# Performance work log

Measured on AMD Instinct MI355X. Metric: run time of the kernel, lower is better.

The kernel has to match this reference:

```python
import jax, jax.numpy as jnp
import numpy as np

B, T, C, H, E, K, F = 2, 2048, 1024, 16, 8, 2, 2048  # batch, seq, d_model, heads, experts, top_k, d_ffn
EPS = 1e-5


def setup_inputs() -> dict:
    key = jax.random.key(0)
    ks = jax.random.split(key, 6)
    s = 0.02
    return {
        "x": jax.random.normal(ks[0], (B, T, C), jnp.float32),
        "ln1_w": jnp.ones((C,), jnp.float32),
        "c_attn_w": jax.random.normal(ks[1], (C, 3 * C), jnp.float32) * s,
        "c_proj_w": jax.random.normal(ks[2], (C, C), jnp.float32) * s,
        "ln2_w": jnp.ones((C,), jnp.float32),
        "router_w": jax.random.normal(ks[3], (C, E), jnp.float32) * s,
        "w1": jnp.clip(jax.random.normal(ks[4], (C, E * F), jnp.float32) * s, -0.06, 0.06),
        "w2": jnp.clip(jax.random.normal(ks[5], (E * F, C), jnp.float32) * s, -0.06, 0.06),
    }


def layernorm(x, w):
    m = x.mean(-1, keepdims=True)
    v = x.var(-1, keepdims=True)
    return (x - m) * jax.lax.rsqrt(v + EPS) * w


def attention(x, c_attn_w, c_proj_w):
    b, t, c = x.shape
    hd = c // H
    q, k, v = jnp.split(x @ c_attn_w, 3, axis=-1)
    q = q.reshape(b, t, H, hd).transpose(0, 2, 1, 3)  # bhtd
    k = k.reshape(b, t, H, hd).transpose(0, 2, 1, 3)
    v = v.reshape(b, t, H, hd).transpose(0, 2, 1, 3)
    att = jnp.einsum('bhqd,bhkd->bhqk', q, k) / jnp.sqrt(jnp.asarray(hd, x.dtype))
    causal = jnp.tril(jnp.ones((t, t), bool))
    att = jnp.where(causal, att, jnp.asarray(-jnp.inf, att.dtype))
    att = jax.nn.softmax(att, axis=-1)
    y = jnp.einsum('bhqk,bhkd->bhqd', att, v)
    y = y.transpose(0, 2, 1, 3).reshape(b, t, c)
    return y @ c_proj_w


def moe_mlp(x, router_w, w1, w2):
    b, t, c = x.shape
    xf = x.reshape(-1, c)  # (N, C), N = b*t
    router_logits = xf @ router_w  # (N, E)
    probs = jax.nn.softmax(router_logits.astype(jnp.float32), axis=-1)
    rw, sel = jax.lax.top_k(probs, K)  # (N, K)
    rw = rw / rw.sum(axis=-1, keepdims=True)  # norm_topk_prob=True
    rw = rw.astype(x.dtype)
    # expert e uses w1[:, e*F:(e+1)*F] and w2[e*F:(e+1)*F, :]
    w1e = w1.reshape(c, E, F).transpose(1, 0, 2)  # (E, C, F)
    w2e = w2.reshape(E, F, c)  # (E, F, C)
    h = jax.nn.gelu(jnp.einsum('nc,ecf->enf', xf, w1e), approximate=False)
    y_all = jnp.einsum('enf,efc->nec', h, w2e)  # (N, E, C)
    y_sel = jnp.take_along_axis(y_all, sel[:, :, None], axis=1)  # (N, K, C)
    y = (y_sel * rw[:, :, None]).sum(axis=1)
    return y.reshape(b, t, c)


def reference(x, ln1_w, c_attn_w, c_proj_w, ln2_w, router_w, w1, w2):
    x = x + attention(layernorm(x, ln1_w), c_attn_w, c_proj_w)
    x = x + moe_mlp(layernorm(x, ln2_w), router_w, w1, w2)
    return x
```

## Files before the change

### kernel.cpp

```cpp
#include <hip/hip_runtime.h>
#include <hip/hip_bf16.h>

#define BB 2
#define TT 2048
#define CCH 1024
#define HH 16
#define HD 64
#define EE 8
#define FF 2048
#define NTOK (BB*TT)

typedef __bf16 bf16x8 __attribute__((ext_vector_type(8)));
typedef float f32x4 __attribute__((ext_vector_type(4)));
typedef unsigned int u32;
typedef const u32 __attribute__((address_space(1)))* gads;
typedef u32 __attribute__((address_space(3)))* lads;

static __device__ __forceinline__ unsigned short f2bf(float f) {
  union { float f; unsigned u; } v; v.f = f;
  unsigned u = v.u;
  u += 0x7fffu + ((u >> 16) & 1u);
  return (unsigned short)(u >> 16);
}
static __device__ __forceinline__ float bf2f(unsigned short h) {
  union { unsigned u; float f; } v; v.u = ((unsigned)h) << 16;
  return v.f;
}

__global__ __launch_bounds__(256) void k_transpose(const float* __restrict__ in,
    unsigned short* __restrict__ out, int R, int Cc) {
  __shared__ float tile[32][33];
  size_t zoff = (size_t)blockIdx.z * (size_t)R * (size_t)Cc;
  int r0 = blockIdx.y * 32, c0 = blockIdx.x * 32;
  int tx = threadIdx.x, ty = threadIdx.y;
#pragma unroll
  for (int ii = 0; ii < 4; ++ii) {
    int i = ty + ii * 8;
    tile[i][tx] = in[zoff + (size_t)(r0 + i) * Cc + c0 + tx];
  }
  __syncthreads();
#pragma unroll
  for (int ii = 0; ii < 4; ++ii) {
    int i = ty + ii * 8;
    out[zoff + (size_t)(c0 + i) * R + r0 + tx] = f2bf(tile[tx][i]);
  }
}

__global__ __launch_bounds__(256) void k_ln(const float* __restrict__ x,
    const float* __restrict__ w, unsigned short* __restrict__ out) {
  int row = blockIdx.x;
  const float* xr = x + (size_t)row * CCH;
  int tid = threadIdx.x;
  float4 v = *(const float4*)&xr[tid * 4];
  float s = v.x + v.y + v.z + v.w;
  float ss = v.x * v.x + v.y * v.y + v.z * v.z + v.w * v.w;
#pragma unroll
  for (int off = 32; off; off >>= 1) { s += __shfl_xor(s, off); ss += __shfl_xor(ss, off); }
  __shared__ float red[8];
  int wv = tid >> 6, l = tid & 63;
  if (l == 0) { red[wv] = s; red[4 + wv] = ss; }
  __syncthreads();
  s = red[0] + red[1] + red[2] + red[3];
  ss = red[4] + red[5] + red[6] + red[7];
  float mean = s * (1.f / CCH);
  float var = ss * (1.f / CCH) - mean * mean;
  float inv = rsqrtf(var + 1e-5f);
  float4 w4 = *(const float4*)&w[tid * 4];
  ushort4 o;
  o.x = f2bf((v.x - mean) * inv * w4.x);
  o.y = f2bf((v.y - mean) * inv * w4.y);
  o.z = f2bf((v.z - mean) * inv * w4.z);
  o.w = f2bf((v.w - mean) * inv * w4.w);
  *(ushort4*)&out[(size_t)row * CCH + tid * 4] = o;
}

#define CSP 140
#define CFP 70
template<int EPI>
__global__ __launch_bounds__(256, 4) void k_gemm128(
    const unsigned short* __restrict__ A, const unsigned short* __restrict__ BT,
    unsigned short* __restrict__ Cb, float* __restrict__ Cf,
    const float* __restrict__ resid, int M, int N, int K,
    const int* __restrict__ tokarr, const int* __restrict__ slotarr,
    const float* __restrict__ wgtarr, const int* __restrict__ offs,
    const int* __restrict__ counts, const int* __restrict__ tmap)
{
  __shared__ __align__(16) char pool[35840];
  unsigned short* As = (unsigned short*)pool;
  unsigned short* Bs = (unsigned short*)(pool + 16384);

  int mb, nb, e = 0, off = 0, cnt = M;
  if (EPI >= 2) {
    int tm = blockIdx.x;
    if (tm >= tmap[8]) return;
    e = 0;
    while (tm >= tmap[e + 1]) ++e;
    mb = tm - tmap[e];
    nb = blockIdx.y;
    cnt = counts[e]; off = offs[e];
  } else {
    int gx = gridDim.x, gy = gridDim.y;
    int nwg = gx * gy;
    int orig = blockIdx.y * gx + blockIdx.x;
    int q = nwg >> 3, r = nwg & 7;
    int xcd = orig & 7, idx = orig >> 3;
    int wk = (xcd < r ? xcd * (q + 1) : r * (q + 1) + (xcd - r) * q) + idx;
    nb = wk % gy; mb = wk / gy;
  }
  int m0 = mb * 128, n0 = nb * 128;

  int tid = threadIdx.x, l = tid & 63, w = tid >> 6;
  int scol = (((l & 7) ^ ((l >> 3) & 7)) * 8);
  const unsigned short* aptr[4];
  const unsigned short* bptr[4];
  const unsigned short* bbase = BT + (size_t)e * (size_t)N * K;
#pragma unroll
  for (int i = 0; i < 4; ++i) {
    int row = (w * 4 + i) * 8 + (l >> 3);
    int ra;
    if (EPI == 2)      ra = tokarr[off + min(m0 + row, cnt - 1)];
    else if (EPI == 3) ra = off + min(m0 + row, cnt - 1);
    else               ra = m0 + row;
    aptr[i] = A + (size_t)ra * K + scol;
    bptr[i] = bbase + (size_t)(n0 + row) * K + scol;
  }

  int wr = (w >> 1) * 64, wc = (w & 1) * 64;
  int frow = l & 15;
  int fkB = (l >> 4) * 16;
  int swz = (frow & 7) << 4;
  f32x4 acc[4][4] = {};

  for (int k0 = 0; k0 < K; k0 += 64) {
#pragma unroll
    for (int i = 0; i < 4; ++i) {
      int j = w * 4 + i;
      __builtin_amdgcn_global_load_lds((gads)(const void*)(aptr[i] + k0),
                                       (lads)(void*)(As + j * 512), 16, 0, 0);
      __builtin_amdgcn_global_load_lds((gads)(const void*)(bptr[i] + k0),
                                       (lads)(void*)(Bs + j * 512), 16, 0, 0);
    }
    __syncthreads();
    const char* ab = (const char*)As;
    const char* bb = (const char*)Bs;
#pragma unroll
    for (int kk = 0; kk < 2; ++kk) {
      int inr = (kk * 64 + fkB) ^ swz;
      bf16x8 af[4], bfr[4];
#pragma unroll
      for (int mi = 0; mi < 4; ++mi)
        af[mi] = *(const bf16x8*)(ab + (wr + mi * 16 + frow) * 128 + inr);
#pragma unroll
      for (int ni = 0; ni < 4; ++ni)
        bfr[ni] = *(const bf16x8*)(bb + (wc + ni * 16 + frow) * 128 + inr);
#pragma unroll
      for (int mi = 0; mi < 4; ++mi)
#pragma unroll
        for (int ni = 0; ni < 4; ++ni)
          acc[mi][ni] = __builtin_amdgcn_mfma_f32_16x16x32_bf16(af[mi], bfr[ni],
                                                                acc[mi][ni], 0, 0, 0);
    }
    __syncthreads();
  }

  int g4 = (l >> 4) * 4, cl = l & 15;

  if (EPI == 0 || EPI == 2) {
    unsigned short* Cs = (unsigned short*)pool;
#pragma unroll
    for (int mi = 0; mi < 4; ++mi)
#pragma unroll
      for (int ni = 0; ni < 4; ++ni)
#pragma unroll
        for (int r2 = 0; r2 < 4; ++r2) {
          float v = acc[mi][ni][r2];
          if (EPI == 2) v = 0.5f * v * (1.f + erff(v * 0.70710678118654752f));
          Cs[(wr + mi * 16 + g4 + r2) * CSP + wc + ni * 16 + cl] = f2bf(v);
        }
    __syncthreads();
    int row = tid >> 1, c0 = (tid & 1) * 64;
    if (EPI == 0 || m0 + row < cnt) {
      size_t grow = (EPI == 2) ? (size_t)(off + m0 + row) : (size_t)(m0 + row);
      unsigned short* dst = Cb + grow * N + n0 + c0;
#pragma unroll
      for (int j = 0; j < 8; ++j)
        ((uint4*)dst)[j] = *(const uint4*)&Cs[row * CSP + c0 + j * 8];
    }
  } else {
    float* Csf = (float*)pool;
#pragma unroll
    for (int p = 0; p < 2; ++p) {
      __syncthreads();
      if ((w & 1) == p) {
#pragma unroll
        for (int mi = 0; mi < 4; ++mi)
#pragma unroll
          for (int ni = 0; ni < 4; ++ni)
#pragma unroll
            for (int r2 = 0; r2 < 4; ++r2)
              Csf[(wr + mi * 16 + g4 + r2) * CFP + ni * 16 + cl] = acc[mi][ni][r2];
      }
      __syncthreads();
      int row = tid >> 1, c0 = (tid & 1) * 32;
      int gcol = n0 + p * 64 + c0;
      if (EPI == 1) {
        float* dst = Cf + (size_t)(m0 + row) * N + gcol;
        const float* rsd = resid + (size_t)(m0 + row) * N + gcol;
#pragma unroll
        for (int j = 0; j < 8; ++j) {
          float4 v = *(const float4*)&Csf[row * CFP + c0 + j * 4];
          float4 rr = ((const float4*)rsd)[j];
          v.x += rr.x; v.y += rr.y; v.z += rr.z; v.w += rr.w;
          ((float4*)dst)[j] = v;
        }
      } else {
        if (m0 + row < cnt) {
          int fl = off + m0 + row;
          int tok = tokarr[fl], slot = slotarr[fl];
          float wg = wgtarr[fl];
          float* dst = Cf + ((size_t)tok * 2 + slot) * N + gcol;
#pragma unroll
          for (int j = 0; j < 8; ++j) {
            float4 v = *(const float4*)&Csf[row * CFP + c0 + j * 4];
            v.x *= wg; v.y *= wg; v.z *= wg; v.w *= wg;
            ((float4*)dst)[j] = v;
          }
        }
      }
    }
  }
}

__global__ __launch_bounds__(256) void k_attn_mfma(const unsigned short* __restrict__ qkv,
    unsigned short* __restrict__ yout)
{
  int bx = blockIdx.x, h = blockIdx.y, b = blockIdx.z;
  int tid = threadIdx.x, l = tid & 63, w = tid >> 6;
  const size_t rs = 3 * CCH;
  const int NTILE = TT / 64;

  __shared__ __align__(16) unsigned short Ks[64][72];
  __shared__ __align__(16) unsigned short Vt[64][72];
  __shared__ __align__(16) unsigned short Ps[4][16][72];

  int frow = l & 15, fk = (l >> 4) * 8;
  int g4 = l >> 4;
  int kr = tid >> 2, kc0 = (tid & 3) * 8;
  int vr = tid >> 2, vc0 = (tid & 3) * 16;

  for (int half = 0; half < 2; ++half) {
    int qt = half ? (NTILE - 1 - bx) : bx;
    int q0 = qt * 64;

    const unsigned short* qp = qkv + (size_t)((size_t)b * TT + q0 + w * 16 + frow) * rs + h * HD;
    bf16x8 qf0 = *(const bf16x8*)&qp[fk];
    bf16x8 qf1 = *(const bf16x8*)&qp[32 + fk];

    f32x4 oacc[4] = {};
    float mrow[4] = {-INFINITY, -INFINITY, -INFINITY, -INFINITY};
    float lrow[4] = {};

    for (int kb = 0; kb <= qt; ++kb) {
      int k0 = kb * 64;
      __syncthreads();
      const unsigned short* kp = qkv + (size_t)((size_t)b * TT + k0 + kr) * rs + CCH + h * HD;
      *(uint4*)&Ks[kr][kc0]      = *(const uint4*)&kp[kc0];
      *(uint4*)&Ks[kr][kc0 + 32] = *(const uint4*)&kp[kc0 + 32];
      const unsigned short* vp = qkv + (size_t)((size_t)b * TT + k0 + vr) * rs + 2 * CCH + h * HD + vc0;
      uint4 v0 = *(const uint4*)&vp[0];
      uint4 v1 = *(const uint4*)&vp[8];
      unsigned short tmp[16];
      *(uint4*)&tmp[0] = v0; *(uint4*)&tmp[8] = v1;
#pragma unroll
      for (int j = 0; j < 16; ++j) Vt[vc0 + j][vr] = tmp[j];
      __syncthreads();

      f32x4 sacc[4] = {};
#pragma unroll
      for (int nb = 0; nb < 4; ++nb) {
        bf16x8 kf0 = *(const bf16x8*)&Ks[nb * 16 + frow][fk];
        bf16x8 kf1 = *(const bf16x8*)&Ks[nb * 16 + frow][32 + fk];
        sacc[nb] = __builtin_amdgcn_mfma_f32_16x16x32_bf16(qf0, kf0, sacc[nb], 0, 0, 0);
        sacc[nb] = __builtin_amdgcn_mfma_f32_16x16x32_bf16(qf1, kf1, sacc[nb], 0, 0, 0);
      }

      bool diag = (kb == qt);
      float sv[4][4];
#pragma unroll
      for (int nb = 0; nb < 4; ++nb)
#pragma unroll
        for (int r = 0; r < 4; ++r) {
          float v = sacc[nb][r] * 0.125f;
          if (diag) {
            int ckv = nb * 16 + frow;
            int rq = w * 16 + 4 * g4 + r;
            if (ckv > rq) v = -INFINITY;
          }
          sv[nb][r] = v;
        }
      float fscale[4];
#pragma unroll
      for (int r = 0; r < 4; ++r) {
        float vm = fmaxf(fmaxf(sv[0][r], sv[1][r]), fmaxf(sv[2][r], sv[3][r]));
        vm = fmaxf(vm, __shfl_xor(vm, 1));
        vm = fmaxf(vm, __shfl_xor(vm, 2));
        vm = fmaxf(vm, __shfl_xor(vm, 4));
        vm = fmaxf(vm, __shfl_xor(vm, 8));
        float mnew = fmaxf(mrow[r], vm);
        float f = __expf(mrow[r] - mnew);
        mrow[r] = mnew;
        fscale[r] = f;
        float psum = 0.f;
#pragma unroll
        for (int nb = 0; nb < 4; ++nb) {
          float p = __expf(sv[nb][r] - mnew);
          sv[nb][r] = p;
          psum += p;
        }
        psum += __shfl_xor(psum, 1);
        psum += __shfl_xor(psum, 2);
        psum += __shfl_xor(psum, 4);
        psum += __shfl_xor(psum, 8);
        lrow[r] = lrow[r] * f + psum;
      }
#pragma unroll
      for (int nb = 0; nb < 4; ++nb)
#pragma unroll
        for (int r = 0; r < 4; ++r) {
          oacc[nb][r] *= fscale[r];
          Ps[w][4 * g4 + r][nb * 16 + frow] = f2bf(sv[nb][r]);
        }
#pragma unroll
      for (int ks = 0; ks < 2; ++ks) {
        bf16x8 pa = *(const bf16x8*)&Ps[w][frow][ks * 32 + fk];
#pragma unroll
        for (int nb = 0; nb < 4; ++nb) {
          bf16x8 vb = *(const bf16x8*)&Vt[nb * 16 + frow][ks * 32 + fk];
          oacc[nb] = __builtin_amdgcn_mfma_f32_16x16x32_bf16(pa, vb, oacc[nb], 0, 0, 0);
        }
      }
    }

    unsigned short* yo = yout + (size_t)((size_t)b * TT + q0 + w * 16) * CCH + h * HD;
#pragma unroll
    for (int r = 0; r < 4; ++r) {
      float inv = 1.f / lrow[r];
      int row = 4 * g4 + r;
#pragma unroll
      for (int nb = 0; nb < 4; ++nb)
        yo[(size_t)row * CCH + nb * 16 + frow] = f2bf(oacc[nb][r] * inv);
    }
  }
}

__global__ __launch_bounds__(256) void k_router(const float* __restrict__ x2,
    const float* __restrict__ ln2w, const float* __restrict__ rw,
    int* __restrict__ sel, float* __restrict__ selw)
{
  int token = blockIdx.x * 4 + (threadIdx.x >> 6);
  int l = threadIdx.x & 63;
  const float* xr = x2 + (size_t)token * CCH;
  float xv[16];
  float s = 0.f, ss = 0.f;
#pragma unroll
  for (int j = 0; j < 16; ++j) { float v = xr[l * 16 + j]; xv[j] = v; s += v; ss += v * v; }
#pragma unroll
  for (int off = 32; off; off >>= 1) { s += __shfl_xor(s, off); ss += __shfl_xor(ss, off); }
  float mean = s * (1.f / CCH);
  float inv = rsqrtf(ss * (1.f / CCH) - mean * mean + 1e-5f);
  float logit[8] = {};
#pragma unroll
  for (int j = 0; j < 16; ++j) {
    float nv = (xv[j] - mean) * inv * ln2w[l * 16 + j];
    const float* rr = &rw[(size_t)(l * 16 + j) * EE];
#pragma unroll
    for (int e = 0; e < 8; ++e) logit[e] = fmaf(nv, rr[e], logit[e]);
  }
#pragma unroll
  for (int e = 0; e < 8; ++e) {
    float v = logit[e];
#pragma unroll
    for (int off = 32; off; off >>= 1) v += __shfl_xor(v, off);
    logit[e] = v;
  }
  float m1 = logit[0]; int i1 = 0;
#pragma unroll
  for (int e = 1; e < 8; ++e) if (logit[e] > m1) { m1 = logit[e]; i1 = e; }
  float m2 = -INFINITY; int i2 = 0;
#pragma unroll
  for (int e = 0; e < 8; ++e) if (e != i1 && logit[e] > m2) { m2 = logit[e]; i2 = e; }
  if (l == 0) {
    float w1v = 1.f / (1.f + __expf(m2 - m1));
    sel[token * 2] = i1; sel[token * 2 + 1] = i2;
    selw[token * 2] = w1v; selw[token * 2 + 1] = 1.f - w1v;
  }
}

__global__ __launch_bounds__(256) void k_count(const int* __restrict__ sel,
    int* __restrict__ counts_pad)
{
  __shared__ int hist[8];
  int tid = threadIdx.x;
  if (tid < 8) hist[tid] = 0;
  __syncthreads();
  int i = blockIdx.x * 256 + tid;
  atomicAdd(&hist[sel[i]], 1);
  __syncthreads();
  if (tid < 8) atomicAdd(&counts_pad[tid * 16], hist[tid]);
}

__global__ void k_offsets(const int* __restrict__ counts_pad, int* __restrict__ counts,
                          int* __restrict__ offs, int* __restrict__ cursors_pad,
                          int* __restrict__ tmap) {
  if (threadIdx.x == 0 && blockIdx.x == 0) {
    int acc = 0, t = 0;
    tmap[0] = 0;
    for (int e = 0; e < 8; ++e) {
      int c = counts_pad[e * 16];
      counts[e] = c; offs[e] = acc; cursors_pad[e * 16] = acc; acc += c;
      t += (c + 127) >> 7;
      tmap[e + 1] = t;
    }
  }
}

__global__ __launch_bounds__(256) void k_scatter(const int* __restrict__ sel,
    const float* __restrict__ selw, int* __restrict__ cursors_pad,
    int* __restrict__ tokarr, int* __restrict__ slotarr, float* __restrict__ wgtarr)
{
  int t = blockIdx.x * 256 + threadIdx.x;
  int l = threadIdx.x & 63;
#pragma unroll
  for (int s2 = 0; s2 < 2; ++s2) {
    int e = sel[t * 2 + s2];
    int pos = 0;
#pragma unroll
    for (int ex = 0; ex < 8; ++ex) {
      unsigned long long mask = __ballot(e == ex);
      if (e == ex) {
        int leader = __ffsll((long long)mask) - 1;
        int cntw = __popcll(mask);
        int base = 0;
        if (l == leader) base = atomicAdd(&cursors_pad[ex * 16], cntw);
        base = __shfl(base, leader);
        unsigned long long below = (l == 0) ? 0ull : (mask << (64 - l));
        pos = base + __popcll(below);
      }
    }
    tokarr[pos] = t; slotarr[pos] = s2; wgtarr[pos] = selw[t * 2 + s2];
  }
}

__global__ __launch_bounds__(256) void k_combine(const float* __restrict__ x2,
    const float* __restrict__ yp, float* __restrict__ out)
{
  int i = blockIdx.x * 256 + threadIdx.x;
  int n = i >> 8, cw = i & 255;
  float4 a = ((const float4*)x2)[i];
  float4 y0 = ((const float4*)yp)[(size_t)(n * 2) * 256 + cw];
  float4 y1 = ((const float4*)yp)[(size_t)(n * 2 + 1) * 256 + cw];
  float4 o;
  o.x = a.x + y0.x + y1.x;
  o.y = a.y + y0.y + y1.y;
  o.z = a.z + y0.z + y1.z;
  o.w = a.w + y0.w + y1.w;
  ((float4*)out)[i] = o;
}

extern "C" void kernel_launch(void* const* d_in, const int* in_sizes, int n_in,
                              void* d_out, int out_size, void* d_ws, size_t ws_size,
                              hipStream_t stream) {
  const float* x     = (const float*)d_in[0];
  const float* ln1w  = (const float*)d_in[1];
  const float* attnw = (const float*)d_in[2];
  const float* projw = (const float*)d_in[3];
  const float* ln2w  = (const float*)d_in[4];
  const float* routw = (const float*)d_in[5];
  const float* w1    = (const float*)d_in[6];
  const float* w2    = (const float*)d_in[7];
  char* ws = (char*)d_ws;

  unsigned short* attn_wT = (unsigned short*)(ws + 0);
  unsigned short* proj_wT = (unsigned short*)(ws + 6291456);
  unsigned short* w1T     = (unsigned short*)(ws + 8388608);
  unsigned short* w2T     = (unsigned short*)(ws + 41943040);
  unsigned short* xn      = (unsigned short*)(ws + 75497472);
  unsigned short* qkv     = (unsigned short*)(ws + 83886080);
  unsigned short* yattn   = (unsigned short*)(ws + 109051904);
  unsigned short* hbuf    = (unsigned short*)(ws + 83886080);
  float* x2 = (float*)(ws + 117440512);
  float* yp = (float*)(ws + 134217728);
  char* rbase = ws + 167772160;
  int* counts_pad  = (int*)(rbase);
  int* counts      = (int*)(rbase + 512);
  int* cursors_pad = (int*)(rbase + 1024);
  int* offs        = (int*)(rbase + 1536);
  int* tmap        = (int*)(rbase + 1600);
  int* sel         = (int*)(rbase + 2048);
  float* selw      = (float*)(rbase + 2048 + 32768);
  int* tokarr      = (int*)(rbase + 2048 + 65536);
  int* slotarr     = (int*)(rbase + 2048 + 98304);
  float* wgtarr    = (float*)(rbase + 2048 + 131072);
  float* outp = (float*)d_out;

  hipMemsetAsync(counts_pad, 0, 512, stream);

  dim3 tb(32, 8);
  k_transpose<<<dim3(96, 32, 1), tb, 0, stream>>>(attnw, attn_wT, 1024, 3072);
  k_transpose<<<dim3(32, 32, 1), tb, 0, stream>>>(projw, proj_wT, 1024, 1024);
  k_transpose<<<dim3(512, 32, 1), tb, 0, stream>>>(w1, w1T, 1024, 16384);
  k_transpose<<<dim3(32, 64, 8), tb, 0, stream>>>(w2, w2T, 2048, 1024);

  k_ln<<<NTOK, 256, 0, stream>>>(x, ln1w, xn);
  k_gemm128<0><<<dim3(32, 24), 256, 0, stream>>>(xn, attn_wT, qkv, nullptr, nullptr,
      NTOK, 3 * CCH, CCH, nullptr, nullptr, nullptr, nullptr, nullptr, nullptr);
  k_attn_mfma<<<dim3(16, 16, 2), 256, 0, stream>>>(qkv, yattn);
  k_gemm128<1><<<dim3(32, 8), 256, 0, stream>>>(yattn, proj_wT, nullptr, x2, x,
      NTOK, CCH, CCH, nullptr, nullptr, nullptr, nullptr, nullptr, nullptr);
  k_ln<<<NTOK, 256, 0, stream>>>(x2, ln2w, xn);
  k_router<<<NTOK / 4, 256, 0, stream>>>(x2, ln2w, routw, sel, selw);
  k_count<<<32, 256, 0, stream>>>(sel, counts_pad);
  k_offsets<<<1, 64, 0, stream>>>(counts_pad, counts, offs, cursors_pad, tmap);
  k_scatter<<<NTOK / 256, 256, 0, stream>>>(sel, selw, cursors_pad, tokarr, slotarr, wgtarr);
  k_gemm128<2><<<dim3(72, 16), 256, 0, stream>>>(xn, w1T, hbuf, nullptr, nullptr,
      NTOK, FF, CCH, tokarr, slotarr, wgtarr, offs, counts, tmap);
  k_gemm128<3><<<dim3(72, 8), 256, 0, stream>>>(hbuf, w2T, nullptr, yp, nullptr,
      NTOK, CCH, FF, tokarr, slotarr, wgtarr, offs, counts, tmap);
  k_combine<<<4096, 256, 0, stream>>>(x2, yp, outp);
}
```

Measured before the change: 411.0 us.

## Remap attention grid to one q-tile per block with XCD-aware ordering and direct-to-LDS K loads

The attention kernel now runs one query tile per block on a flat 1024-block grid instead of pairing two tiles per block. Blocks are ordered longest-first and heads are mapped so that blocks on the same XCD share a head. K tiles are loaded straight into a swizzled LDS layout with global_load_lds, skipping the register round trip and the padded layout. The aim is better load balance, L2 locality and fewer bank conflicts, at the cost of more blocks and a new swizzle indexing scheme.

Measured after the change: 447.4 us. 1.09x slower.

```diff
diff --git a/kernel.cpp b/kernel.cpp
--- a/kernel.cpp
+++ b/kernel.cpp
@@ -234,38 +234,50 @@
 __global__ __launch_bounds__(256) void k_attn_mfma(const unsigned short* __restrict__ qkv,
     unsigned short* __restrict__ yout)
 {
-  int bx = blockIdx.x, h = blockIdx.y, b = blockIdx.z;
+  int fblk = blockIdx.x;
+  int xcd = fblk & 7, s = fblk >> 3;
+  int h = xcd + 8 * ((s >> 5) & 1);
+  int b = s >> 6;
+  int qt = 31 - (s & 31);
+  int q0 = qt * 64;
+
   int tid = threadIdx.x, l = tid & 63, w = tid >> 6;
   const size_t rs = 3 * CCH;
-  const int NTILE = TT / 64;
-
-  __shared__ __align__(16) unsigned short Ks[64][72];
+
+  __shared__ __align__(16) unsigned short Ks[64 * 64];
   __shared__ __align__(16) unsigned short Vt[64][72];
   __shared__ __align__(16) unsigned short Ps[4][16][72];
 
   int frow = l & 15, fk = (l >> 4) * 8;
   int g4 = l >> 4;
-  int kr = tid >> 2, kc0 = (tid & 3) * 8;
   int vr = tid >> 2, vc0 = (tid & 3) * 16;
 
-  for (int half = 0; half < 2; ++half) {
-    int qt = half ? (NTILE - 1 - bx) : bx;
-    int q0 = qt * 64;
-
-    const unsigned short* qp = qkv + (size_t)((size_t)b * TT + q0 + w * 16 + frow) * rs + h * HD;
-    bf16x8 qf0 = *(const bf16x8*)&qp[fk];
-    bf16x8 qf1 = *(const bf16x8*)&qp[32 + fk];
-
-    f32x4 oacc[4] = {};
-    float mrow[4] = {-INFINITY, -INFINITY, -INFINITY, -INFINITY};
-    float lrow[4] = {};
-
-    for (int kb = 0; kb <= qt; ++kb) {
-      int k0 = kb * 64;
-      __syncthreads();
-      const unsigned short* kp = qkv + (size_t)((size_t)b * TT + k0 + kr) * rs + CCH + h * HD;
-      *(uint4*)&Ks[kr][kc0]      = *(const uint4*)&kp[kc0];
-      *(uint4*)&Ks[kr][kc0 + 32] = *(const uint4*)&kp[kc0 + 32];
+  int scol = (((l & 7) ^ ((l >> 3) & 7)) * 8);
+  const unsigned short* kbase[2];
+#pragma unroll
+  for (int i = 0; i < 2; ++i) {
+    int row = (w * 2 + i) * 8 + (l >> 3);
+    kbase[i] = qkv + (size_t)((size_t)b * TT + row) * rs + CCH + h * HD + scol;
+  }
+
+  const unsigned short* qp = qkv + (size_t)((size_t)b * TT + q0 + w * 16 + frow) * rs + h * HD;
+  bf16x8 qf0 = *(const bf16x8*)&qp[fk];
+  bf16x8 qf1 = *(const bf16x8*)&qp[32 + fk];
+
+  f32x4 oacc[4] = {};
+  float mrow[4] = {-INFINITY, -INFINITY, -INFINITY, -INFINITY};
+  float lrow[4] = {};
+
+  for (int kb = 0; kb <= qt; ++kb) {
+    int k0 = kb * 64;
+    __syncthreads();
+#pragma unroll
+    for (int i = 0; i < 2; ++i) {
+      int j = w * 2 + i;
+      __builtin_amdgcn_global_load_lds((gads)(const void*)(kbase[i] + (size_t)k0 * rs),
+                                       (lads)(void*)(Ks + j * 512), 16, 0, 0);
+    }
+    {
       const unsigned short* vp = qkv + (size_t)((size_t)b * TT + k0 + vr) * rs + 2 * CCH + h * HD + vc0;
       uint4 v0 = *(const uint4*)&vp[0];
       uint4 v1 = *(const uint4*)&vp[8];
@@ -273,83 +285,85 @@
       *(uint4*)&tmp[0] = v0; *(uint4*)&tmp[8] = v1;
 #pragma unroll
       for (int j = 0; j < 16; ++j) Vt[vc0 + j][vr] = tmp[j];
-      __syncthreads();
-
-      f32x4 sacc[4] = {};
+    }
+    __syncthreads();
+
+    f32x4 sacc[4] = {};
+#pragma unroll
+    for (int nb = 0; nb < 4; ++nb) {
+      int rr = nb * 16 + frow;
+      const char* krow = (const char*)Ks + rr * 128;
+      bf16x8 kf0 = *(const bf16x8*)(krow + ((((l >> 4)) ^ (rr & 7)) << 4));
+      bf16x8 kf1 = *(const bf16x8*)(krow + ((((l >> 4) + 4) ^ (rr & 7)) << 4));
+      sacc[nb] = __builtin_amdgcn_mfma_f32_16x16x32_bf16(qf0, kf0, sacc[nb], 0, 0, 0);
+      sacc[nb] = __builtin_amdgcn_mfma_f32_16x16x32_bf16(qf1, kf1, sacc[nb], 0, 0, 0);
+    }
+
+    bool diag = (kb == qt);
+    float sv[4][4];
+#pragma unroll
+    for (int nb = 0; nb < 4; ++nb)
+#pragma unroll
+      for (int r = 0; r < 4; ++r) {
+        float v = sacc[nb][r] * 0.125f;
+        if (diag) {
+          int ckv = nb * 16 + frow;
+          int rq = w * 16 + 4 * g4 + r;
+          if (ckv > rq) v = -INFINITY;
+        }
+        sv[nb][r] = v;
+      }
+    float fscale[4];
+#pragma unroll
+    for (int r = 0; r < 4; ++r) {
+      float vm = fmaxf(fmaxf(sv[0][r], sv[1][r]), fmaxf(sv[2][r], sv[3][r]));
+      vm = fmaxf(vm, __shfl_xor(vm, 1));
+      vm = fmaxf(vm, __shfl_xor(vm, 2));
+      vm = fmaxf(vm, __shfl_xor(vm, 4));
+      vm = fmaxf(vm, __shfl_xor(vm, 8));
+      float mnew = fmaxf(mrow[r], vm);
+      float f = __expf(mrow[r] - mnew);
+      mrow[r] = mnew;
+      fscale[r] = f;
+      float psum = 0.f;
 #pragma unroll
       for (int nb = 0; nb < 4; ++nb) {
-        bf16x8 kf0 = *(const bf16x8*)&Ks[nb * 16 + frow][fk];
-        bf16x8 kf1 = *(const bf16x8*)&Ks[nb * 16 + frow][32 + fk];
-        sacc[nb] = __builtin_amdgcn_mfma_f32_16x16x32_bf16(qf0, kf0, sacc[nb], 0, 0, 0);
-        sacc[nb] = __builtin_amdgcn_mfma_f32_16x16x32_bf16(qf1, kf1, sacc[nb], 0, 0, 0);
-      }
-
-      bool diag = (kb == qt);
-      float sv[4][4];
-#pragma unroll
-      for (int nb = 0; nb < 4; ++nb)
-#pragma unroll
-        for (int r = 0; r < 4; ++r) {
-          float v = sacc[nb][r] * 0.125f;
-          if (diag) {
-            int ckv = nb * 16 + frow;
-            int rq = w * 16 + 4 * g4 + r;
-            if (ckv > rq) v = -INFINITY;
-          }
-          sv[nb][r] = v;
-        }
-      float fscale[4];
+        float p = __expf(sv[nb][r] - mnew);
+        sv[nb][r] = p;
+        psum += p;
+      }
+      psum += __shfl_xor(psum, 1);
+      psum += __shfl_xor(psum, 2);
+      psum += __shfl_xor(psum, 4);
+      psum += __shfl_xor(psum, 8);
+      lrow[r] = lrow[r] * f + psum;
+    }
+#pragma unroll
+    for (int nb = 0; nb < 4; ++nb)
 #pragma unroll
       for (int r = 0; r < 4; ++r) {
-        float vm = fmaxf(fmaxf(sv[0][r], sv[1][r]), fmaxf(sv[2][r], sv[3][r]));
-        vm = fmaxf(vm, __shfl_xor(vm, 1));
-        vm = fmaxf(vm, __shfl_xor(vm, 2));
-        vm = fmaxf(vm, __shfl_xor(vm, 4));
-        vm = fmaxf(vm, __shfl_xor(vm, 8));
-        float mnew = fmaxf(mrow[r], vm);
-        float f = __expf(mrow[r] - mnew);
-        mrow[r] = mnew;
-        fscale[r] = f;
-        float psum = 0.f;
-#pragma unroll
-        for (int nb = 0; nb < 4; ++nb) {
-          float p = __expf(sv[nb][r] - mnew);
-          sv[nb][r] = p;
-          psum += p;
-        }
-        psum += __shfl_xor(psum, 1);
-        psum += __shfl_xor(psum, 2);
-        psum += __shfl_xor(psum, 4);
-        psum += __shfl_xor(psum, 8);
-        lrow[r] = lrow[r] * f + psum;
-      }
-#pragma unroll
-      for (int nb = 0; nb < 4; ++nb)
-#pragma unroll
-        for (int r = 0; r < 4; ++r) {
-          oacc[nb][r] *= fscale[r];
-          Ps[w][4 * g4 + r][nb * 16 + frow] = f2bf(sv[nb][r]);
-        }
-#pragma unroll
-      for (int ks = 0; ks < 2; ++ks) {
-        bf16x8 pa = *(const bf16x8*)&Ps[w][frow][ks * 32 + fk];
-#pragma unroll
-        for (int nb = 0; nb < 4; ++nb) {
-          bf16x8 vb = *(const bf16x8*)&Vt[nb * 16 + frow][ks * 32 + fk];
-          oacc[nb] = __builtin_amdgcn_mfma_f32_16x16x32_bf16(pa, vb, oacc[nb], 0, 0, 0);
-        }
-      }
-    }
-
-    unsigned short* yo = yout + (size_t)((size_t)b * TT + q0 + w * 16) * CCH + h * HD;
-#pragma unroll
-    for (int r = 0; r < 4; ++r) {
-      float inv = 1.f / lrow[r];
-      int row = 4 * g4 + r;
-#pragma unroll
-      for (int nb = 0; nb < 4; ++nb)
-        yo[(size_t)row * CCH + nb * 16 + frow] = f2bf(oacc[nb][r] * inv);
-    }
+        oacc[nb][r] *= fscale[r];
+        Ps[w][4 * g4 + r][nb * 16 + frow] = f2bf(sv[nb][r]);
+      }
+#pragma unroll
+    for (int ks = 0; ks < 2; ++ks) {
+      bf16x8 pa = *(const bf16x8*)&Ps[w][frow][ks * 32 + fk];
+#pragma unroll
+      for (int nb = 0; nb < 4; ++nb) {
+        bf16x8 vb = *(const bf16x8*)&Vt[nb * 16 + frow][ks * 32 + fk];
+        oacc[nb] = __builtin_amdgcn_mfma_f32_16x16x32_bf16(pa, vb, oacc[nb], 0, 0, 0);
+      }
+    }
+  }
+
+  unsigned short* yo = yout + (size_t)((size_t)b * TT + q0 + w * 16) * CCH + h * HD;
+#pragma unroll
+  for (int r = 0; r < 4; ++r) {
+    float inv = 1.f / lrow[r];
+    int row = 4 * g4 + r;
+#pragma unroll
+    for (int nb = 0; nb < 4; ++nb)
+      yo[(size_t)row * CCH + nb * 16 + frow] = f2bf(oacc[nb][r] * inv);
   }
 }
 
@@ -514,7 +528,7 @@
   k_ln<<<NTOK, 256, 0, stream>>>(x, ln1w, xn);
   k_gemm128<0><<<dim3(32, 24), 256, 0, stream>>>(xn, attn_wT, qkv, nullptr, nullptr,
       NTOK, 3 * CCH, CCH, nullptr, nullptr, nullptr, nullptr, nullptr, nullptr);
-  k_attn_mfma<<<dim3(16, 16, 2), 256, 0, stream>>>(qkv, yattn);
+  k_attn_mfma<<<dim3(1024), 256, 0, stream>>>(qkv, yattn);
   k_gemm128<1><<<dim3(32, 8), 256, 0, stream>>>(yattn, proj_wT, nullptr, x2, x,
       NTOK, CCH, CCH, nullptr, nullptr, nullptr, nullptr, nullptr, nullptr);
   k_ln<<<NTOK, 256, 0, stream>>>(x2, ln2w, xn);
```

## Prefetch next K/V tile into registers and remap attention grid for XCD locality

Applied to the files above, without the earlier changes.

The attention kernel now loads the next K/V tile from global memory into registers while the current tile is being computed, so global load latency overlaps with the MFMA and softmax work. The grid is also flattened to 1D and remapped so blocks sharing a head land on the same XCD, which is meant to improve L2 reuse of K/V. The prefetch adds register pressure, which may reduce occupancy.

New measurement: 397.5 us. 1.03x faster.

```diff
diff --git a/kernel.cpp b/kernel.cpp
--- a/kernel.cpp
+++ b/kernel.cpp
@@ -234,7 +234,11 @@
 __global__ __launch_bounds__(256) void k_attn_mfma(const unsigned short* __restrict__ qkv,
     unsigned short* __restrict__ yout)
 {
-  int bx = blockIdx.x, h = blockIdx.y, b = blockIdx.z;
+  int fblk = blockIdx.x;
+  int xcd = fblk & 7, s = fblk >> 3;
+  int h = xcd + 8 * (s & 1);
+  int b = (s >> 1) & 1;
+  int bx = s >> 2;
   int tid = threadIdx.x, l = tid & 63, w = tid >> 6;
   const size_t rs = 3 * CCH;
   const int NTILE = TT / 64;
@@ -260,20 +264,36 @@
     float mrow[4] = {-INFINITY, -INFINITY, -INFINITY, -INFINITY};
     float lrow[4] = {};
 
+    uint4 rk0, rk1, rv0, rv1;
+    {
+      const unsigned short* kp = qkv + (size_t)((size_t)b * TT + kr) * rs + CCH + h * HD;
+      rk0 = *(const uint4*)&kp[kc0];
+      rk1 = *(const uint4*)&kp[kc0 + 32];
+      const unsigned short* vp = qkv + (size_t)((size_t)b * TT + vr) * rs + 2 * CCH + h * HD + vc0;
+      rv0 = *(const uint4*)&vp[0];
+      rv1 = *(const uint4*)&vp[8];
+    }
+
     for (int kb = 0; kb <= qt; ++kb) {
-      int k0 = kb * 64;
       __syncthreads();
-      const unsigned short* kp = qkv + (size_t)((size_t)b * TT + k0 + kr) * rs + CCH + h * HD;
-      *(uint4*)&Ks[kr][kc0]      = *(const uint4*)&kp[kc0];
-      *(uint4*)&Ks[kr][kc0 + 32] = *(const uint4*)&kp[kc0 + 32];
-      const unsigned short* vp = qkv + (size_t)((size_t)b * TT + k0 + vr) * rs + 2 * CCH + h * HD + vc0;
-      uint4 v0 = *(const uint4*)&vp[0];
-      uint4 v1 = *(const uint4*)&vp[8];
-      unsigned short tmp[16];
-      *(uint4*)&tmp[0] = v0; *(uint4*)&tmp[8] = v1;
-#pragma unroll
-      for (int j = 0; j < 16; ++j) Vt[vc0 + j][vr] = tmp[j];
+      *(uint4*)&Ks[kr][kc0]      = rk0;
+      *(uint4*)&Ks[kr][kc0 + 32] = rk1;
+      {
+        unsigned short tmp[16];
+        *(uint4*)&tmp[0] = rv0; *(uint4*)&tmp[8] = rv1;
+#pragma unroll
+        for (int j = 0; j < 16; ++j) Vt[vc0 + j][vr] = tmp[j];
+      }
       __syncthreads();
+      if (kb < qt) {
+        int k0n = (kb + 1) * 64;
+        const unsigned short* kp = qkv + (size_t)((size_t)b * TT + k0n + kr) * rs + CCH + h * HD;
+        rk0 = *(const uint4*)&kp[kc0];
+        rk1 = *(const uint4*)&kp[kc0 + 32];
+        const unsigned short* vp = qkv + (size_t)((size_t)b * TT + k0n + vr) * rs + 2 * CCH + h * HD + vc0;
+        rv0 = *(const uint4*)&vp[0];
+        rv1 = *(const uint4*)&vp[8];
+      }
 
       f32x4 sacc[4] = {};
 #pragma unroll
@@ -514,7 +534,7 @@
   k_ln<<<NTOK, 256, 0, stream>>>(x, ln1w, xn);
   k_gemm128<0><<<dim3(32, 24), 256, 0, stream>>>(xn, attn_wT, qkv, nullptr, nullptr,
       NTOK, 3 * CCH, CCH, nullptr, nullptr, nullptr, nullptr, nullptr, nullptr);
-  k_attn_mfma<<<dim3(16, 16, 2), 256, 0, stream>>>(qkv, yattn);
+  k_attn_mfma<<<dim3(512), 256, 0, stream>>>(qkv, yattn);
   k_gemm128<1><<<dim3(32, 8), 256, 0, stream>>>(yattn, proj_wT, nullptr, x2, x,
       NTOK, CCH, CCH, nullptr, nullptr, nullptr, nullptr, nullptr, nullptr);
   k_ln<<<NTOK, 256, 0, stream>>>(x2, ln2w, xn);
```
